# Kernel optimization log

Hardware: AMD Instinct MI355X
Metric: run time of the kernel (lower is better)

Reference implementation:

```python
import jax, jax.numpy as jnp
import numpy as np

EPS = 1e-5

def _proj(x, w, b, gamma, beta, mean, var):
    # 1x1 conv (einsum over channels) + BatchNorm (inference) ; Dropout is identity in eval.
    y = jnp.einsum('bchw,oc->bohw', x, w) + b[None, :, None, None]
    scale = gamma * jax.lax.rsqrt(var + EPS)
    shift = beta - mean * scale
    return y * scale[None, :, None, None] + shift[None, :, None, None]

def _make_layer(key, cin, cout):
    k1, k2, k3, k4 = jax.random.split(key, 4)
    w = jax.random.normal(k1, (cout, cin), jnp.float32) * (1.0 / np.sqrt(cin))
    b = jax.random.normal(k2, (cout,), jnp.float32) * 0.01
    gamma = 1.0 + 0.1 * jax.random.normal(k3, (cout,), jnp.float32)
    beta = 0.1 * jax.random.normal(k4, (cout,), jnp.float32)
    mean = 0.05 * jax.random.normal(jax.random.fold_in(k1, 7), (cout,), jnp.float32)
    var = 0.5 + jax.random.uniform(jax.random.fold_in(k2, 7), (cout,), jnp.float32)
    return w, b, gamma, beta, mean, var

def setup_inputs() -> dict:
    key = jax.random.key(0)
    B, C, Ci, H, W = 4, 128, 64, 64, 64
    ks = jax.random.split(key, 6)
    inp = {
        'x1': jax.random.normal(ks[0], (B, C, H, W), jnp.float32),
        'x2': jax.random.normal(ks[1], (B, C, H, W), jnp.float32),
    }
    for name, k, cin, cout in [('theta', ks[2], C, Ci), ('phi', ks[3], C, Ci),
                               ('g', ks[4], C, Ci), ('wout', ks[5], Ci, C)]:
        w, b, gm, bt, mn, vr = _make_layer(k, cin, cout)
        inp.update({f'{name}_w': w, f'{name}_b': b, f'{name}_g': gm,
                    f'{name}_beta': bt, f'{name}_m': mn, f'{name}_v': vr})
    return inp

def reference(x1, x2,
              theta_w, theta_b, theta_g, theta_beta, theta_m, theta_v,
              phi_w, phi_b, phi_g, phi_beta, phi_m, phi_v,
              g_w, g_b, g_g, g_beta, g_m, g_v,
              wout_w, wout_b, wout_g, wout_beta, wout_m, wout_v):
    B, C, H, W = x1.shape
    N = H * W
    theta_x1 = _proj(x1, theta_w, theta_b, theta_g, theta_beta, theta_m, theta_v).reshape(B, -1, N)  # [B,Ci,N]
    phi_x2 = _proj(x2, phi_w, phi_b, phi_g, phi_beta, phi_m, phi_v).reshape(B, -1, N)                # [B,Ci,N]
    g_x2 = _proj(x2, g_w, g_b, g_g, g_beta, g_m, g_v).reshape(B, -1, N)                              # [B,Ci,N]
    # attention_map[b, n, m] = sum_c theta[b,c,n] * phi[b,c,m]
    attn = jax.nn.softmax(jnp.einsum('bcn,bcm->bnm', theta_x1, phi_x2), axis=-1)  # [B,N,N]
    out = jnp.einsum('bnm,bcm->bcn', attn, g_x2).reshape(B, -1, H, W)             # [B,Ci,H,W]
    out = _proj(out, wout_w, wout_b, wout_g, wout_beta, wout_m, wout_v)           # [B,C,H,W]
    return jnp.concatenate((out, x1), axis=1)                                     # [B,2C,H,W]
```

## Files before the change

kernel.cpp:

```cpp
#include <hip/hip_runtime.h>
#include <stdint.h>
#include <stddef.h>

#define EPS   1e-5f
#define CINCH 128
#define CI    64
#define NPIX  4096
#define KSPL  8
#define LOG2E 1.44269504088896340736f

typedef __bf16 bf16_t;
typedef _Float16 f16_t;
typedef bf16_t bf16x8 __attribute__((ext_vector_type(8)));
typedef f16_t  f16x8  __attribute__((ext_vector_type(8)));
typedef float  f32x4  __attribute__((ext_vector_type(4)));

typedef __attribute__((address_space(3))) unsigned int lds_u32;
typedef __attribute__((address_space(1))) const unsigned int glb_u32;

__device__ __forceinline__ f32x4 mfma16(bf16x8 a, bf16x8 b, f32x4 c) {
  return __builtin_amdgcn_mfma_f32_16x16x32_bf16(a, b, c, 0, 0, 0);
}
__device__ __forceinline__ f32x4 fzero4() {
  f32x4 z = {0.f, 0.f, 0.f, 0.f};
  return z;
}
__device__ __forceinline__ void gload16(const void* g, void* l) {
  __builtin_amdgcn_global_load_lds((glb_u32*)g, (lds_u32*)l, 16, 0, 0);
}


__global__ __launch_bounds__(256) void proj_theta(
    const float* __restrict__ x1,
    const float* __restrict__ w,  const float* __restrict__ bb,
    const float* __restrict__ gm, const float* __restrict__ bt,
    const float* __restrict__ mn, const float* __restrict__ vr,
    bf16_t* __restrict__ thetaT_h, bf16_t* __restrict__ thetaT_l,
    float* __restrict__ out)
{
  __shared__ float wT[CINCH][CI];
  __shared__ float bfold[CI];
  __shared__ __align__(16) char ubuf[CINCH * 32 * 4];
  float (*xs)[32]    = (float(*)[32])ubuf;
  float (*tileF)[68] = (float(*)[68])ubuf;

  const int tid = threadIdx.x;
  const int b   = blockIdx.y;
  const int n0  = blockIdx.x * 32;

  for (int idx = tid; idx < CI * CINCH; idx += 256) {
    const int o = idx & 63, c = idx >> 6;
    const float sc = gm[o] * rsqrtf(vr[o] + EPS);
    wT[c][o] = w[o * CINCH + c] * sc * LOG2E;
    if (c == 0) bfold[o] = (bb[o] * sc + bt[o] - mn[o] * sc) * LOG2E;
  }

  {
    const float* xsrc = x1 + (size_t)b * CINCH * NPIX + n0;
    float* osrc = out + ((size_t)b * 256 + 128) * NPIX + n0;
#pragma unroll
    for (int i = 0; i < 4; ++i) {
      const int idx = i * 256 + tid;
      const int c = idx >> 3, p = idx & 7;
      const f32x4 v = *(const f32x4*)(xsrc + (size_t)c * NPIX + p * 4);
      *(f32x4*)&xs[c][p * 4] = v;
      *(f32x4*)(osrc + (size_t)c * NPIX + p * 4) = v;
    }
  }
  __syncthreads();

  const int px = tid & 31;
  const int og = tid >> 5;
  float acc[8];
#pragma unroll
  for (int j = 0; j < 8; ++j) acc[j] = 0.f;

#pragma unroll 4
  for (int c0 = 0; c0 < CINCH; c0 += 4) {
    float xv[4];
#pragma unroll
    for (int cc = 0; cc < 4; ++cc) xv[cc] = xs[c0 + cc][px];
#pragma unroll
    for (int cc = 0; cc < 4; ++cc) {
      const f32x4 w0 = *(const f32x4*)&wT[c0 + cc][og * 8];
      const f32x4 w1 = *(const f32x4*)&wT[c0 + cc][og * 8 + 4];
#pragma unroll
      for (int j = 0; j < 4; ++j) {
        acc[j]     += w0[j] * xv[cc];
        acc[j + 4] += w1[j] * xv[cc];
      }
    }
  }
  __syncthreads();
#pragma unroll
  for (int j = 0; j < 8; ++j) tileF[px][og * 8 + j] = acc[j] + bfold[og * 8 + j];
  __syncthreads();

  {
    const int px2 = tid >> 3, ogs = tid & 7;
    bf16x8 hv, lv;
#pragma unroll
    for (int j = 0; j < 8; ++j) {
      const float v = tileF[px2][ogs * 8 + j];
      const bf16_t h = (bf16_t)v;
      hv[j] = h;
      lv[j] = (bf16_t)(v - (float)h);
    }
    const size_t base = ((size_t)b * NPIX + n0 + px2) * CI + ogs * 8;
    *(bf16x8*)(thetaT_h + base) = hv;
    *(bf16x8*)(thetaT_l + base) = lv;
  }
}

__global__ __launch_bounds__(256) void proj_phi(
    const float* __restrict__ x2,
    const float* __restrict__ w,  const float* __restrict__ bb,
    const float* __restrict__ gm, const float* __restrict__ bt,
    const float* __restrict__ mn, const float* __restrict__ vr,
    bf16_t* __restrict__ phiT_h, bf16_t* __restrict__ phiT_l)
{
  __shared__ float wT[CINCH][CI];
  __shared__ float bfold[CI];
  __shared__ __align__(16) char ubuf[CINCH * 32 * 4];
  float (*xs)[32]    = (float(*)[32])ubuf;
  float (*tileF)[68] = (float(*)[68])ubuf;

  const int tid = threadIdx.x;
  const int b   = blockIdx.y;
  const int n0  = blockIdx.x * 32;

  for (int idx = tid; idx < CI * CINCH; idx += 256) {
    const int o = idx & 63, c = idx >> 6;
    const float sc = gm[o] * rsqrtf(vr[o] + EPS);
    wT[c][o] = w[o * CINCH + c] * sc;
    if (c == 0) bfold[o] = bb[o] * sc + bt[o] - mn[o] * sc;
  }
  {
    const float* xsrc = x2 + (size_t)b * CINCH * NPIX + n0;
#pragma unroll
    for (int i = 0; i < 4; ++i) {
      const int idx = i * 256 + tid;
      const int c = idx >> 3, p = idx & 7;
      *(f32x4*)&xs[c][p * 4] = *(const f32x4*)(xsrc + (size_t)c * NPIX + p * 4);
    }
  }
  __syncthreads();

  const int px = tid & 31;
  const int og = tid >> 5;
  float acc[8];
#pragma unroll
  for (int j = 0; j < 8; ++j) acc[j] = 0.f;

#pragma unroll 4
  for (int c0 = 0; c0 < CINCH; c0 += 4) {
    float xv[4];
#pragma unroll
    for (int cc = 0; cc < 4; ++cc) xv[cc] = xs[c0 + cc][px];
#pragma unroll
    for (int cc = 0; cc < 4; ++cc) {
      const f32x4 w0 = *(const f32x4*)&wT[c0 + cc][og * 8];
      const f32x4 w1 = *(const f32x4*)&wT[c0 + cc][og * 8 + 4];
#pragma unroll
      for (int j = 0; j < 4; ++j) {
        acc[j]     += w0[j] * xv[cc];
        acc[j + 4] += w1[j] * xv[cc];
      }
    }
  }
  __syncthreads();
#pragma unroll
  for (int j = 0; j < 8; ++j) tileF[px][og * 8 + j] = acc[j] + bfold[og * 8 + j];
  __syncthreads();

  {
    const int px2 = tid >> 3, ogs = tid & 7;
    const int n = n0 + px2;
    bf16x8 hv, lv;
#pragma unroll
    for (int j = 0; j < 8; ++j) {
      const float v = tileF[px2][ogs * 8 + j];
      const bf16_t h = (bf16_t)v;
      hv[j] = h;
      lv[j] = (bf16_t)(v - (float)h);
    }
    const size_t rowb = ((size_t)b * NPIX + n) * 128;
    const int byte = (ogs * 16) ^ ((n & 7) << 4);
    *(bf16x8*)((char*)phiT_h + rowb + byte) = hv;
    *(bf16x8*)((char*)phiT_l + rowb + byte) = lv;
  }
}

__global__ __launch_bounds__(256) void proj_g(
    const float* __restrict__ x2,
    const float* __restrict__ w,  const float* __restrict__ bb,
    const float* __restrict__ gm, const float* __restrict__ bt,
    const float* __restrict__ mn, const float* __restrict__ vr,
    bf16_t* __restrict__ g_cm)
{
  __shared__ float wT[CINCH][CI];
  __shared__ float bfold[CI];
  __shared__ __align__(16) char ubuf[CINCH * 32 * 4];
  float (*xs)[32] = (float(*)[32])ubuf;
  float (*gT)[33] = (float(*)[33])ubuf;

  const int tid = threadIdx.x;
  const int b   = blockIdx.y;
  const int n0  = blockIdx.x * 32;

  for (int idx = tid; idx < CI * CINCH; idx += 256) {
    const int o = idx & 63, c = idx >> 6;
    const float sc = gm[o] * rsqrtf(vr[o] + EPS);
    wT[c][o] = w[o * CINCH + c] * sc;
    if (c == 0) bfold[o] = bb[o] * sc + bt[o] - mn[o] * sc;
  }
  {
    const float* xsrc = x2 + (size_t)b * CINCH * NPIX + n0;
#pragma unroll
    for (int i = 0; i < 4; ++i) {
      const int idx = i * 256 + tid;
      const int c = idx >> 3, p = idx & 7;
      *(f32x4*)&xs[c][p * 4] = *(const f32x4*)(xsrc + (size_t)c * NPIX + p * 4);
    }
  }
  __syncthreads();

  const int px = tid & 31;
  const int og = tid >> 5;
  float acc[8];
#pragma unroll
  for (int j = 0; j < 8; ++j) acc[j] = 0.f;

#pragma unroll 4
  for (int c0 = 0; c0 < CINCH; c0 += 4) {
    float xv[4];
#pragma unroll
    for (int cc = 0; cc < 4; ++cc) xv[cc] = xs[c0 + cc][px];
#pragma unroll
    for (int cc = 0; cc < 4; ++cc) {
      const f32x4 w0 = *(const f32x4*)&wT[c0 + cc][og * 8];
      const f32x4 w1 = *(const f32x4*)&wT[c0 + cc][og * 8 + 4];
#pragma unroll
      for (int j = 0; j < 4; ++j) {
        acc[j]     += w0[j] * xv[cc];
        acc[j + 4] += w1[j] * xv[cc];
      }
    }
  }
  __syncthreads();
#pragma unroll
  for (int j = 0; j < 8; ++j) gT[og * 8 + j][px] = acc[j] + bfold[og * 8 + j];
  __syncthreads();

  {
    const int c = tid & 63, mgp = tid >> 6;
    bf16x8 gv;
#pragma unroll
    for (int j = 0; j < 8; ++j) gv[j] = (bf16_t)gT[c][mgp * 8 + j];
    *(bf16x8*)(g_cm + ((size_t)b * CI + c) * NPIX + n0 + mgp * 8) = gv;
  }
}

__global__ __launch_bounds__(512, 4) void flash_attn(
    const bf16_t* __restrict__ thetaT_h, const bf16_t* __restrict__ thetaT_l,
    const bf16_t* __restrict__ phiT_h,   const bf16_t* __restrict__ phiT_l,
    const bf16_t* __restrict__ g_cm,
    f16_t* __restrict__ Opart, float* __restrict__ mlbuf)
{
  __shared__ __attribute__((aligned(16))) char sK[2][16384];
  __shared__ __attribute__((aligned(16))) char sV[2][8192];
  __shared__ __attribute__((aligned(16))) char sP[8][4096];

  const int tid  = threadIdx.x;
  const int lane = tid & 63;
  const int wid  = tid >> 6;
  const int lrow = lane & 15;
  const int lhi  = lane >> 4;

  const int wg = blockIdx.x;
  const int b  = wg >> 7;
  const int rr = wg & 127;
  const int qt = rr >> 3;
  const int ks = rr & 7;
  const int q0 = qt * 256 + wid * 32;
  const int tg0 = ks * 8;

  const char* const srcPHb = (const char*)phiT_h + ((size_t)b * NPIX) * 128;
  const char* const srcPLb = (const char*)phiT_l + ((size_t)b * NPIX) * 128;
  const char* const srcVb  = (const char*)g_cm + (size_t)b * CI * NPIX * 2;

  const int vc = tid >> 3, vp = tid & 7;

  auto stageK = [&](int buf, int tg) {
    const size_t rb = (size_t)tg * 8192;
    gload16(srcPHb + rb + tid * 16, sK[buf] + tid * 16);
    gload16(srcPLb + rb + tid * 16, sK[buf] + 8192 + tid * 16);
  };
  auto loadV = [&](int tg) {
    return *(const f32x4*)(srcVb + ((size_t)vc * NPIX + tg * 64 + vp * 8) * 2);
  };
  auto writeV = [&](int buf, f32x4 v) {
    *(f32x4*)(sV[buf] + vc * 128 + ((vp * 16) ^ ((vc & 7) << 4))) = v;
  };

  bf16x8 qh[2][2], qlv[2][2];
  {
    const bf16_t* qbh = thetaT_h + ((size_t)b * NPIX + q0 + lrow) * CI + lhi * 8;
    const bf16_t* qbl = thetaT_l + ((size_t)b * NPIX + q0 + lrow) * CI + lhi * 8;
#pragma unroll
    for (int nt = 0; nt < 2; ++nt)
#pragma unroll
      for (int kk = 0; kk < 2; ++kk) {
        qh[nt][kk]  = *(const bf16x8*)(qbh + nt * 16 * CI + kk * 32);
        qlv[nt][kk] = *(const bf16x8*)(qbl + nt * 16 * CI + kk * 32);
      }
  }

  f32x4 oacc[2][4];
#pragma unroll
  for (int a = 0; a < 2; ++a)
#pragma unroll
    for (int c = 0; c < 4; ++c) oacc[a][c] = fzero4();

  float m_run[2] = {-1e30f, -1e30f};
  float l_run[2] = {0.f, 0.f};

  char* const Pw = sP[wid];
  const int pswz[2] = {(lrow & 7) << 4, ((lrow & 7) << 4)};

  stageK(0, tg0);
  writeV(0, loadV(tg0));
  __syncthreads();

  for (int t = 0; t < 8; ++t) {
    const int cur = t & 1;
    const bool more = (t < 7);
    f32x4 vnext;
    if (more) { stageK(cur ^ 1, tg0 + t + 1); vnext = loadV(tg0 + t + 1); }

    const char* const sKH = sK[cur];
    const char* const sKL = sK[cur] + 8192;

    f32x4 s[4][2];
#pragma unroll
    for (int mt = 0; mt < 4; ++mt)
#pragma unroll
      for (int nt = 0; nt < 2; ++nt) s[mt][nt] = fzero4();

    __builtin_amdgcn_s_setprio(1);
#pragma unroll
    for (int mt = 0; mt < 4; ++mt) {
      const int row = mt * 16 + lrow;
      const int swz = (row & 7) << 4;
#pragma unroll
      for (int kk = 0; kk < 2; ++kk) {
        const int byte = row * 128 + ((kk * 64 + lhi * 16) ^ swz);
        const bf16x8 aH = *(const bf16x8*)(sKH + byte);
        const bf16x8 aL = *(const bf16x8*)(sKL + byte);
#pragma unroll
        for (int nt = 0; nt < 2; ++nt) {
          s[mt][nt] = mfma16(aH, qh[nt][kk],  s[mt][nt]);
          s[mt][nt] = mfma16(aH, qlv[nt][kk], s[mt][nt]);
          s[mt][nt] = mfma16(aL, qh[nt][kk],  s[mt][nt]);
        }
      }
    }
    __builtin_amdgcn_s_setprio(0);

    float mx[2], a2[2];
#pragma unroll
    for (int nt = 0; nt < 2; ++nt) {
      float m1 = fmaxf(fmaxf(s[0][nt][0], s[0][nt][1]), fmaxf(s[0][nt][2], s[0][nt][3]));
      float m2 = fmaxf(fmaxf(s[1][nt][0], s[1][nt][1]), fmaxf(s[1][nt][2], s[1][nt][3]));
      float m3 = fmaxf(fmaxf(s[2][nt][0], s[2][nt][1]), fmaxf(s[2][nt][2], s[2][nt][3]));
      float m4 = fmaxf(fmaxf(s[3][nt][0], s[3][nt][1]), fmaxf(s[3][nt][2], s[3][nt][3]));
      float m = fmaxf(fmaxf(m1, m2), fmaxf(m3, m4));
      m = fmaxf(m, __shfl_xor(m, 16));
      m = fmaxf(m, __shfl_xor(m, 32));
      mx[nt] = m;
    }
    const bool up = !__all((mx[0] <= m_run[0]) && (mx[1] <= m_run[1]));
#pragma unroll
    for (int nt = 0; nt < 2; ++nt) {
      const float mnew  = up ? fmaxf(m_run[nt], mx[nt]) : m_run[nt];
      const float alpha = up ? exp2f(m_run[nt] - mnew) : 1.f;
      float lsum = 0.f;
#pragma unroll
      for (int mt = 0; mt < 4; ++mt)
#pragma unroll
        for (int r = 0; r < 4; ++r) {
          const float p = exp2f(s[mt][nt][r] - mnew);
          s[mt][nt][r] = p;
          lsum += p;
        }
      lsum += __shfl_xor(lsum, 16);
      lsum += __shfl_xor(lsum, 32);
      l_run[nt] = l_run[nt] * alpha + lsum;
      m_run[nt] = mnew;
      a2[nt] = alpha;
    }

    if (up) {
#pragma unroll
      for (int qt2 = 0; qt2 < 2; ++qt2) {
#pragma unroll
        for (int r = 0; r < 4; ++r) {
          const float av = __shfl(a2[qt2], lhi * 4 + r);
#pragma unroll
          for (int ct = 0; ct < 4; ++ct) oacc[qt2][ct][r] *= av;
        }
      }
    }

#pragma unroll
    for (int mt = 0; mt < 4; ++mt)
#pragma unroll
      for (int nt = 0; nt < 2; ++nt) {
        union { bf16_t h[4]; uint32_t u[2]; } pk;
#pragma unroll
        for (int r = 0; r < 4; ++r) pk.h[r] = (bf16_t)s[mt][nt][r];
        const int q    = nt * 16 + lrow;
        const int mloc = mt * 16 + lhi * 4;
        const int byte = q * 128 + ((mloc * 2) ^ ((q & 7) << 4));
        *(uint2*)(Pw + byte) = make_uint2(pk.u[0], pk.u[1]);
      }

    if (more) writeV(cur ^ 1, vnext);

    const char* const sVc = sV[cur];
    bf16x8 bV[2][4];
#pragma unroll
    for (int ct = 0; ct < 4; ++ct) {
      const int row = ct * 16 + lrow;
      const int swz = (row & 7) << 4;
#pragma unroll
      for (int kk = 0; kk < 2; ++kk)
        bV[kk][ct] = *(const bf16x8*)(sVc + row * 128 + ((kk * 64 + lhi * 16) ^ swz));
    }
    __builtin_amdgcn_s_setprio(1);
#pragma unroll
    for (int qt2 = 0; qt2 < 2; ++qt2) {
      const int q = qt2 * 16 + lrow;
#pragma unroll
      for (int kk = 0; kk < 2; ++kk) {
        const bf16x8 pfrag =
            *(const bf16x8*)(Pw + q * 128 + ((kk * 64 + lhi * 16) ^ ((q & 7) << 4)));
#pragma unroll
        for (int ct = 0; ct < 4; ++ct)
          oacc[qt2][ct] = mfma16(pfrag, bV[kk][ct], oacc[qt2][ct]);
      }
    }
    __builtin_amdgcn_s_setprio(0);

    if (more) __syncthreads();
  }

  f16_t* const Ob = Opart + ((size_t)(b * KSPL + ks) * NPIX) * 64;
#pragma unroll
  for (int qt2 = 0; qt2 < 2; ++qt2)
#pragma unroll
    for (int ct = 0; ct < 4; ++ct)
#pragma unroll
      for (int r = 0; r < 4; ++r) {
        const int q = q0 + qt2 * 16 + lhi * 4 + r;
        const int c = ct * 16 + lrow;
        Ob[(size_t)q * 64 + c] = (f16_t)oacc[qt2][ct][r];
      }
  if (lhi < 2) {
    const int q = q0 + lhi * 16 + lrow;
    const size_t base = ((size_t)(b * KSPL + ks) * NPIX + q) * 2;
    mlbuf[base]     = m_run[lhi];
    mlbuf[base + 1] = l_run[lhi];
  }
}

__global__ __launch_bounds__(256) void merge_out(
    const f16_t* __restrict__ Opart, const float* __restrict__ mlbuf,
    const float* __restrict__ ww,  const float* __restrict__ wb,
    const float* __restrict__ wg,  const float* __restrict__ wbt,
    const float* __restrict__ wm,  const float* __restrict__ wvv,
    float* __restrict__ out)
{
  __shared__ float wlds[128][64];
  __shared__ float bfw[128];
  __shared__ float mrg[32][68];

  const int tid = threadIdx.x;
  const int b   = blockIdx.y;
  const int n0  = blockIdx.x * 32;

  for (int idx = tid; idx < 128 * 64; idx += 256) {
    const int o = idx >> 6, c = idx & 63;
    const float sc = wg[o] * rsqrtf(wvv[o] + EPS);
    wlds[o][c] = ww[o * 64 + c] * sc;
    if (c == 0) bfw[o] = wb[o] * sc + wbt[o] - wm[o] * sc;
  }

  {
    const int px = tid & 31;
    const int cg = tid >> 5;
    const int q  = n0 + px;
    float mk[KSPL], lk[KSPL];
#pragma unroll
    for (int ks = 0; ks < KSPL; ++ks) {
      const size_t base = ((size_t)(b * KSPL + ks) * NPIX + q) * 2;
      mk[ks] = mlbuf[base];
      lk[ks] = mlbuf[base + 1];
    }
    float M = mk[0];
#pragma unroll
    for (int ks = 1; ks < KSPL; ++ks) M = fmaxf(M, mk[ks]);
    float al[KSPL]; float den = 0.f;
#pragma unroll
    for (int ks = 0; ks < KSPL; ++ks) { al[ks] = exp2f(mk[ks] - M); den += al[ks] * lk[ks]; }
    const float inv = 1.f / den;
#pragma unroll
    for (int ks = 0; ks < KSPL; ++ks) al[ks] *= inv;

    float r[8];
#pragma unroll
    for (int j = 0; j < 8; ++j) r[j] = 0.f;
#pragma unroll
    for (int ks = 0; ks < KSPL; ++ks) {
      const f16x8 p = *(const f16x8*)(Opart +
          ((size_t)(b * KSPL + ks) * NPIX + q) * 64 + cg * 8);
#pragma unroll
      for (int j = 0; j < 8; ++j) r[j] += (float)p[j] * al[ks];
    }
#pragma unroll
    for (int j = 0; j < 8; ++j) mrg[px][cg * 8 + j] = r[j];
  }
  __syncthreads();

  const int px = tid & 31;
  const int oh = tid >> 5;
  float acc[16];
#pragma unroll
  for (int j = 0; j < 16; ++j) acc[j] = 0.f;

#pragma unroll 4
  for (int c0 = 0; c0 < 64; c0 += 4) {
    const f32x4 m4 = *(const f32x4*)&mrg[px][c0];
#pragma unroll
    for (int j = 0; j < 16; ++j) {
      const f32x4 w4 = *(const f32x4*)&wlds[oh * 16 + j][c0];
      acc[j] += w4[0] * m4[0] + w4[1] * m4[1] + w4[2] * m4[2] + w4[3] * m4[3];
    }
  }
#pragma unroll
  for (int j = 0; j < 16; ++j) {
    const int o = oh * 16 + j;
    out[((size_t)b * 256 + o) * NPIX + n0 + px] = acc[j] + bfw[o];
  }
}

extern "C" void kernel_launch(void* const* d_in, const int* in_sizes, int n_in,
                              void* d_out, int out_size, void* d_ws, size_t ws_size,
                              hipStream_t stream) {
  (void)in_sizes; (void)n_in; (void)out_size; (void)ws_size;
  const float* x1  = (const float*)d_in[0];
  const float* x2  = (const float*)d_in[1];
  const float* tw  = (const float*)d_in[2];
  const float* tb  = (const float*)d_in[3];
  const float* tg  = (const float*)d_in[4];
  const float* tbt = (const float*)d_in[5];
  const float* tm  = (const float*)d_in[6];
  const float* tv  = (const float*)d_in[7];
  const float* pw  = (const float*)d_in[8];
  const float* pb  = (const float*)d_in[9];
  const float* pg  = (const float*)d_in[10];
  const float* pbt = (const float*)d_in[11];
  const float* pm  = (const float*)d_in[12];
  const float* pv  = (const float*)d_in[13];
  const float* gw  = (const float*)d_in[14];
  const float* gb  = (const float*)d_in[15];
  const float* gg  = (const float*)d_in[16];
  const float* gbt = (const float*)d_in[17];
  const float* gmn = (const float*)d_in[18];
  const float* gv  = (const float*)d_in[19];
  const float* ww  = (const float*)d_in[20];
  const float* wb  = (const float*)d_in[21];
  const float* wg  = (const float*)d_in[22];
  const float* wbt = (const float*)d_in[23];
  const float* wm  = (const float*)d_in[24];
  const float* wv  = (const float*)d_in[25];

  float* out = (float*)d_out;
  char*  ws  = (char*)d_ws;
  bf16_t* thetaT_h = (bf16_t*)(ws);
  bf16_t* thetaT_l = (bf16_t*)(ws + (size_t)(2)  * 1048576);
  bf16_t* phiT_h   = (bf16_t*)(ws + (size_t)(4)  * 1048576);
  bf16_t* phiT_l   = (bf16_t*)(ws + (size_t)(6)  * 1048576);
  bf16_t* g_cm     = (bf16_t*)(ws + (size_t)(8)  * 1048576);
  f16_t*  Opart    = (f16_t*) (ws + (size_t)(10) * 1048576);
  float*  mlbuf    = (float*) (ws + (size_t)(26) * 1048576);

  dim3 gp(128, 4);
  proj_theta<<<gp, 256, 0, stream>>>(x1, tw, tb, tg, tbt, tm, tv,
                                     thetaT_h, thetaT_l, out);
  proj_phi<<<gp, 256, 0, stream>>>(x2, pw, pb, pg, pbt, pm, pv,
                                   phiT_h, phiT_l);
  proj_g<<<gp, 256, 0, stream>>>(x2, gw, gb, gg, gbt, gmn, gv, g_cm);
  flash_attn<<<512, 512, 0, stream>>>(thetaT_h, thetaT_l, phiT_h, phiT_l,
                                      g_cm, Opart, mlbuf);
  merge_out<<<gp, 256, 0, stream>>>(Opart, mlbuf, ww, wb, wg, wbt, wm, wv, out);
}
```

Measured before the change: 249.8 us.

## Stage V tiles with async global-to-LDS loads and stage output through LDS

V tiles are now loaded with the same direct global-to-LDS async loads as the K tiles, in place of register loads followed by LDS writes, so one stage call prefetches K and V together. The loop synchronisation is rebuilt around explicit vmcnt/lgkmcnt waits and raw barriers. The online-softmax rescale now fires only when the new max exceeds the running max by more than 5, which skips more rescales but lets exponents grow up to 2^5 before rescaling. The final partial output is transposed through the per-wave LDS buffer so it can be written with coalesced 16-byte stores instead of scattered 2-byte stores.

```diff
diff --git a/kernel.cpp b/kernel.cpp
--- a/kernel.cpp
+++ b/kernel.cpp
@@ -290,18 +290,16 @@
   const char* const srcVb  = (const char*)g_cm + (size_t)b * CI * NPIX * 2;
 
   const int vc = tid >> 3, vp = tid & 7;
-
-  auto stageK = [&](int buf, int tg) {
+  const size_t vsrcoff = (size_t)vc * (NPIX * 2) + ((vp * 16) ^ ((vc & 7) << 4));
+
+  auto stage = [&](int buf, int tg) {
     const size_t rb = (size_t)tg * 8192;
     gload16(srcPHb + rb + tid * 16, sK[buf] + tid * 16);
     gload16(srcPLb + rb + tid * 16, sK[buf] + 8192 + tid * 16);
+    gload16(srcVb + vsrcoff + (size_t)tg * 128, sV[buf] + tid * 16);
   };
-  auto loadV = [&](int tg) {
-    return *(const f32x4*)(srcVb + ((size_t)vc * NPIX + tg * 64 + vp * 8) * 2);
-  };
-  auto writeV = [&](int buf, f32x4 v) {
-    *(f32x4*)(sV[buf] + vc * 128 + ((vp * 16) ^ ((vc & 7) << 4))) = v;
-  };
+
+  stage(0, tg0);
 
   bf16x8 qh[2][2], qlv[2][2];
   {
@@ -326,20 +324,28 @@
   float l_run[2] = {0.f, 0.f};
 
   char* const Pw = sP[wid];
-  const int pswz[2] = {(lrow & 7) << 4, ((lrow & 7) << 4)};
-
-  stageK(0, tg0);
-  writeV(0, loadV(tg0));
+
   __syncthreads();
 
   for (int t = 0; t < 8; ++t) {
     const int cur = t & 1;
-    const bool more = (t < 7);
-    f32x4 vnext;
-    if (more) { stageK(cur ^ 1, tg0 + t + 1); vnext = loadV(tg0 + t + 1); }
+
+    if (t) {
+      asm volatile("s_waitcnt lgkmcnt(0)" ::: "memory");
+      __builtin_amdgcn_s_barrier();
+    }
+    if (t < 7) {
+      stage(cur ^ 1, tg0 + t + 1);
+      asm volatile("s_waitcnt vmcnt(3)" ::: "memory");
+    } else {
+      asm volatile("s_waitcnt vmcnt(0)" ::: "memory");
+    }
+    __builtin_amdgcn_s_barrier();
+    __builtin_amdgcn_sched_barrier(0);
 
     const char* const sKH = sK[cur];
     const char* const sKL = sK[cur] + 8192;
+    const char* const sVc = sV[cur];
 
     f32x4 s[4][2];
 #pragma unroll
@@ -379,7 +385,7 @@
       m = fmaxf(m, __shfl_xor(m, 32));
       mx[nt] = m;
     }
-    const bool up = !__all((mx[0] <= m_run[0]) && (mx[1] <= m_run[1]));
+    const bool up = !__all((mx[0] <= m_run[0] + 5.f) && (mx[1] <= m_run[1] + 5.f));
 #pragma unroll
     for (int nt = 0; nt < 2; ++nt) {
       const float mnew  = up ? fmaxf(m_run[nt], mx[nt]) : m_run[nt];
@@ -425,9 +431,6 @@
         *(uint2*)(Pw + byte) = make_uint2(pk.u[0], pk.u[1]);
       }
 
-    if (more) writeV(cur ^ 1, vnext);
-
-    const char* const sVc = sV[cur];
     bf16x8 bV[2][4];
 #pragma unroll
     for (int ct = 0; ct < 4; ++ct) {
@@ -451,21 +454,26 @@
       }
     }
     __builtin_amdgcn_s_setprio(0);
-
-    if (more) __syncthreads();
-  }
-
-  f16_t* const Ob = Opart + ((size_t)(b * KSPL + ks) * NPIX) * 64;
-#pragma unroll
-  for (int qt2 = 0; qt2 < 2; ++qt2)
-#pragma unroll
-    for (int ct = 0; ct < 4; ++ct)
-#pragma unroll
-      for (int r = 0; r < 4; ++r) {
-        const int q = q0 + qt2 * 16 + lhi * 4 + r;
-        const int c = ct * 16 + lrow;
-        Ob[(size_t)q * 64 + c] = (f16_t)oacc[qt2][ct][r];
-      }
+  }
+
+  {
+#pragma unroll
+    for (int qt2 = 0; qt2 < 2; ++qt2)
+#pragma unroll
+      for (int ct = 0; ct < 4; ++ct)
+#pragma unroll
+        for (int r = 0; r < 4; ++r) {
+          const int ql = qt2 * 16 + lhi * 4 + r;
+          const int c  = ct * 16 + lrow;
+          *(f16_t*)(Pw + (ql * 64 + c) * 2) = (f16_t)oacc[qt2][ct][r];
+        }
+    f16_t* const Ob = Opart + ((size_t)(b * KSPL + ks) * NPIX + q0) * 64;
+#pragma unroll
+    for (int i = 0; i < 4; ++i) {
+      const int idx = i * 64 + lane;
+      *(f16x8*)(Ob + idx * 8) = *(const f16x8*)(Pw + idx * 16);
+    }
+  }
   if (lhi < 2) {
     const int q = q0 + lhi * 16 + lrow;
     const size_t base = ((size_t)(b * KSPL + ks) * NPIX + q) * 2;
```

Result: no change. 249.3 us (-0.2%).
